# Optimization experiments

Measured on AMD Instinct MI355X. Metric: run time of the kernel, lower is better.

The kernel has to match this reference:

```python
import jax, jax.numpy as jnp
import numpy as np

N, E = 50000, 800000
D_IN, D_HID, D_OUT = 128, 256, 128


def setup_inputs() -> dict:
    key = jax.random.key(0)
    k = jax.random.split(key, 7)
    x = jax.random.normal(k[0], (N, D_IN), dtype=jnp.float32)
    edge_src = jax.random.randint(k[1], (E,), 0, N, dtype=jnp.int32)
    edge_dst = jax.random.randint(k[2], (E,), 0, N, dtype=jnp.int32)
    s1 = 1.0 / np.sqrt(2 * D_IN)
    s2 = 1.0 / np.sqrt(2 * D_HID)
    W1 = jax.random.uniform(k[3], (2 * D_IN, D_HID), jnp.float32, -s1, s1)
    b1 = jax.random.uniform(k[4], (D_HID,), jnp.float32, -s1, s1)
    W2 = jax.random.uniform(k[5], (2 * D_HID, D_OUT), jnp.float32, -s2, s2)
    b2 = jax.random.uniform(k[6], (D_OUT,), jnp.float32, -s2, s2)
    return {"x": x, "edge_src": edge_src, "edge_dst": edge_dst,
            "W1": W1, "b1": b1, "W2": W2, "b2": b2}


def _sage_layer(h, edge_src, edge_dst, W, b, inv_deg):
    # mean-pool neighbor features: gather [E, D] then segment-sum to [N, D]
    msgs = h[edge_src]
    agg = jax.ops.segment_sum(msgs, edge_dst, num_segments=h.shape[0]) * inv_deg
    y = jnp.concatenate([h, agg], axis=1)  # [N, 2D]
    return y @ W + b


def reference(x, edge_src, edge_dst, W1, b1, W2, b2):
    n = x.shape[0]
    deg = jax.ops.segment_sum(jnp.ones_like(edge_dst, dtype=x.dtype), edge_dst,
                              num_segments=n)
    inv_deg = (1.0 / jnp.maximum(deg, 1.0))[:, None]  # isolated nodes -> zeros
    h = _sage_layer(x, edge_src, edge_dst, W1, b1, inv_deg)
    h = jax.nn.relu(h)
    # dropout is identity in eval mode
    h = _sage_layer(h, edge_src, edge_dst, W2, b2, inv_deg)
    return jax.nn.log_softmax(h, axis=1)
```

## Files before the change

kernel.cpp:

```cpp
#include <hip/hip_runtime.h>
#include <cstdint>
#include <cstddef>

typedef __attribute__((ext_vector_type(8))) short bf16x8;
typedef __attribute__((ext_vector_type(4))) float f32x4;
typedef __attribute__((ext_vector_type(2))) float f32x2;

__device__ inline short bf16_rne(float f) {
  unsigned u = __builtin_bit_cast(unsigned, f);
  u += 0x7fff + ((u >> 16) & 1);
  return (short)(u >> 16);
}

__device__ inline float bf16lo(unsigned v) { return __builtin_bit_cast(float, v << 16); }
__device__ inline float bf16hi(unsigned v) { return __builtin_bit_cast(float, v & 0xffff0000u); }

__device__ inline unsigned pack2(float a, float b) {
  return ((unsigned)(unsigned short)bf16_rne(a)) | (((unsigned)(unsigned short)bf16_rne(b)) << 16);
}


__global__ __launch_bounds__(256) void prep_kernel(const float* __restrict__ W1,
                                                   const float* __restrict__ W2,
                                                   const float* __restrict__ b2,
                                                   const float* __restrict__ x,
                                                   short* __restrict__ B1p,
                                                   short* __restrict__ B2p,
                                                   float* __restrict__ bias2,
                                                   unsigned* __restrict__ A1u,
                                                   unsigned* __restrict__ xf8, int nquads,
                                                   int* __restrict__ counters, int NB) {
  int b = blockIdx.x;
  int tid = threadIdx.x;
  int nqb = (nquads + 255) >> 8;
  if (b < 512) {
    int mode = b >> 8;
    int idx = (b & 255) * 256 + tid;
    int j = idx & 7;
    int L = (idx >> 3) & 63;
    int nt = (idx >> 9) & 15;
    int kb = idx >> 13;
    int k = kb * 32 + (L >> 4) * 8 + j;
    int n = nt * 16 + (L & 15);
    if (mode == 0) {
      B1p[idx] = bf16_rne(W1[(size_t)k * 256 + n]);
    } else {
      float v = (n < 128) ? W2[(size_t)k * 128 + n] : W2[(size_t)(256 + k) * 128 + (n - 128)];
      B2p[idx] = bf16_rne(v);
    }
  } else if (b == 512) {
    bias2[tid] = (tid < 128) ? b2[tid] : 0.0f;
  } else if (b < 513 + nqb) {
    int idx = (b - 513) * 256 + tid;
    if (idx < nquads) {
      int n = idx >> 5, q = idx & 31;
      float4 v = ((const float4*)x)[idx];
      ((uint2*)A1u)[(size_t)n * 64 + q] = make_uint2(pack2(v.x, v.y), pack2(v.z, v.w));
      int pk = __builtin_amdgcn_cvt_pk_fp8_f32(v.x, v.y, 0, false);
      pk = __builtin_amdgcn_cvt_pk_fp8_f32(v.z, v.w, pk, true);
      xf8[(size_t)n * 32 + q] = (unsigned)pk;
    }
  } else {
    for (int t = tid; t < NB; t += 256) counters[t] = 0;
  }
}

__global__ __launch_bounds__(256) void bucket_scatter(const int* __restrict__ src,
                                                      const int* __restrict__ dst, int E, int EPB,
                                                      int* __restrict__ counters, int NB,
                                                      int SLACK, unsigned* __restrict__ bedge) {
  __shared__ int h[512];
  __shared__ int base[512];
  int tid = threadIdx.x;
  for (int t = tid; t < NB; t += 256) h[t] = 0;
  __syncthreads();
  int start = blockIdx.x * EPB, end = min(E, start + EPB);
  for (int i = start + tid; i < end; i += 256) atomicAdd(&h[((unsigned)dst[i]) >> 7], 1);
  __syncthreads();
  for (int t = tid; t < NB; t += 256) {
    int c = h[t];
    base[t] = (c > 0) ? atomicAdd(&counters[t], c) : 0;
    h[t] = 0;
  }
  __syncthreads();
  for (int i = start + tid; i < end; i += 256) {
    unsigned d = (unsigned)dst[i];
    unsigned bk = d >> 7;
    int p = base[bk] + atomicAdd(&h[bk], 1);
    bedge[(size_t)bk * SLACK + p] = ((d & 127u) << 24) | (unsigned)src[i];
  }
}

__global__ __launch_bounds__(256) void build_csr(const unsigned* __restrict__ bedge,
                                                 const int* __restrict__ counters,
                                                 int NB, int SLACK, int N,
                                                 int* __restrict__ offsets,
                                                 int* __restrict__ oend,
                                                 float* __restrict__ inv_deg,
                                                 int* __restrict__ ssrc) {
  __shared__ int buf[128];
  int b = blockIdx.x, tid = threadIdx.x;
  int cntE = counters[b];
  int rb = b * SLACK;
  if (tid < 128) buf[tid] = 0;
  __syncthreads();
  for (int i = tid; i < cntE; i += 256) atomicAdd(&buf[bedge[(size_t)rb + i] >> 24], 1);
  __syncthreads();
  int cnt = (tid < 128) ? buf[tid] : 0;
  #pragma unroll
  for (int off = 1; off < 128; off <<= 1) {
    int t = (tid >= off && tid < 128) ? buf[tid - off] : 0;
    __syncthreads();
    if (tid < 128) buf[tid] += t;
    __syncthreads();
  }
  if (tid < 128) {
    int excl_l = buf[tid] - cnt;
    int node = (b << 7) + tid;
    if (node < N) {
      offsets[node] = rb + excl_l;
      oend[node]    = rb + excl_l + cnt;
      inv_deg[node] = 1.0f / fmaxf((float)cnt, 1.0f);
    }
    buf[tid] = rb + excl_l;
  }
  __syncthreads();
  for (int i = tid; i < cntE; i += 256) {
    unsigned e2 = bedge[(size_t)rb + i];
    int p = atomicAdd(&buf[e2 >> 24], 1);
    ssrc[p] = (int)(e2 & 0xFFFFFFu);
  }
}

#define CVT8(U, A0, A1, A2, A3, A4, A5, A6, A7)                                        \
  {                                                                                    \
    f32x2 p_, q_;                                                                      \
    p_ = __builtin_amdgcn_cvt_pk_f32_fp8((U).x, false);                                \
    q_ = __builtin_amdgcn_cvt_pk_f32_fp8((U).x, true);                                 \
    A0 += p_[0]; A1 += p_[1]; A2 += q_[0]; A3 += q_[1];                                \
    p_ = __builtin_amdgcn_cvt_pk_f32_fp8((U).y, false);                                \
    q_ = __builtin_amdgcn_cvt_pk_f32_fp8((U).y, true);                                 \
    A4 += p_[0]; A5 += p_[1]; A6 += q_[0]; A7 += q_[1];                                \
  }

__global__ __launch_bounds__(256) void agg1_kernel(const uint2* __restrict__ X8,
                                                   const int* __restrict__ offsets,
                                                   const int* __restrict__ oend,
                                                   const int* __restrict__ ssrc,
                                                   const float* __restrict__ inv_deg,
                                                   uint4* __restrict__ A1q, int N) {
  int node = blockIdx.x * 4 + (threadIdx.x >> 6);
  if (node >= N) return;
  int lane = threadIdx.x & 63;
  int g = lane >> 4;
  int l = lane & 15;
  int s = offsets[node], e = oend[node];
  float a0=0.f,a1=0.f,a2=0.f,a3=0.f,a4=0.f,a5=0.f,a6=0.f,a7=0.f;
  int i = s;
  for (; i + 16 <= e; i += 16) {
    int sA = ssrc[i + g], sB = ssrc[i + 4 + g];
    int sC = ssrc[i + 8 + g], sD = ssrc[i + 12 + g];
    uint2 u = X8[((size_t)(unsigned)sA << 4) + l];
    uint2 v = X8[((size_t)(unsigned)sB << 4) + l];
    uint2 w = X8[((size_t)(unsigned)sC << 4) + l];
    uint2 z = X8[((size_t)(unsigned)sD << 4) + l];
    CVT8(u, a0,a1,a2,a3,a4,a5,a6,a7);
    CVT8(v, a0,a1,a2,a3,a4,a5,a6,a7);
    CVT8(w, a0,a1,a2,a3,a4,a5,a6,a7);
    CVT8(z, a0,a1,a2,a3,a4,a5,a6,a7);
  }
  for (; i < e; i += 4) {
    if (g < e - i) {
      uint2 u = X8[((size_t)(unsigned)ssrc[i + g] << 4) + l];
      CVT8(u, a0,a1,a2,a3,a4,a5,a6,a7);
    }
  }
  a0 += __shfl_xor(a0,16,64); a0 += __shfl_xor(a0,32,64);
  a1 += __shfl_xor(a1,16,64); a1 += __shfl_xor(a1,32,64);
  a2 += __shfl_xor(a2,16,64); a2 += __shfl_xor(a2,32,64);
  a3 += __shfl_xor(a3,16,64); a3 += __shfl_xor(a3,32,64);
  a4 += __shfl_xor(a4,16,64); a4 += __shfl_xor(a4,32,64);
  a5 += __shfl_xor(a5,16,64); a5 += __shfl_xor(a5,32,64);
  a6 += __shfl_xor(a6,16,64); a6 += __shfl_xor(a6,32,64);
  a7 += __shfl_xor(a7,16,64); a7 += __shfl_xor(a7,32,64);
  if (g == 0) {
    float id = inv_deg[node];
    A1q[((size_t)node << 5) + 16 + l] =
        make_uint4(pack2(a0 * id, a1 * id), pack2(a2 * id, a3 * id),
                   pack2(a4 * id, a5 * id), pack2(a6 * id, a7 * id));
  }
}

__global__ __launch_bounds__(256, 2) void gemm_mfma(const short* __restrict__ A,
                                                    const short* __restrict__ Bp,
                                                    const float* __restrict__ bias,
                                                    void* __restrict__ out0,
                                                    void* __restrict__ out1,
                                                    int S, int mode) {
  int tid = threadIdx.x;
  int w = tid >> 6;
  int lane = tid & 63;

  bf16x8 breg[8][4];
  #pragma unroll
  for (int kb = 0; kb < 8; ++kb)
    #pragma unroll
    for (int j = 0; j < 4; ++j)
      breg[kb][j] = *(const bf16x8*)(Bp + ((size_t)((kb * 16 + w * 4 + j) * 64 + lane)) * 8);

  float bj[4];
  #pragma unroll
  for (int j = 0; j < 4; ++j) bj[j] = bias[w * 64 + j * 16 + (lane & 15)];

  int rowInFrag = lane & 15;
  int kseg = (lane >> 4) * 8;

  for (int s = blockIdx.x; s < S; s += gridDim.x) {
    int row0 = s * 16;
    const short* Arow = A + (size_t)(row0 + rowInFrag) * 256 + kseg;
    bf16x8 afr[8];
    #pragma unroll
    for (int kb = 0; kb < 8; ++kb) afr[kb] = *(const bf16x8*)(Arow + kb * 32);

    f32x4 acc[4];
    #pragma unroll
    for (int j = 0; j < 4; ++j) acc[j] = (f32x4)(0.0f);
    #pragma unroll
    for (int kb = 0; kb < 8; ++kb)
      #pragma unroll
      for (int j = 0; j < 4; ++j)
        acc[j] = __builtin_amdgcn_mfma_f32_16x16x32_bf16(afr[kb], breg[kb][j], acc[j], 0, 0, 0);

    int crow0 = row0 + (lane >> 4) * 4;
    int ccol = lane & 15;
    #pragma unroll
    for (int j = 0; j < 4; ++j) {
      int col = w * 64 + j * 16 + ccol;
      #pragma unroll
      for (int r = 0; r < 4; ++r) {
        float v = acc[j][r] + bj[j];
        int row = crow0 + r;
        if (mode == 0) {
          ((short*)out0)[(size_t)row * 256 + col] = bf16_rne(fmaxf(v, 0.0f));
        } else if (w < 2) {
          ((short*)out0)[(size_t)row * 128 + col] = bf16_rne(v);
        } else {
          int pk = __builtin_amdgcn_cvt_pk_fp8_f32(v, v, 0, false);
          ((unsigned char*)out1)[(size_t)row * 128 + (col - 128)] = (unsigned char)(pk & 0xff);
        }
      }
    }
  }
}

__global__ __launch_bounds__(256) void final_kernel(const uint4* __restrict__ utopq,
                                                    const uint2* __restrict__ T2,
                                                    const int* __restrict__ offsets,
                                                    const int* __restrict__ oend,
                                                    const int* __restrict__ ssrc,
                                                    const float* __restrict__ inv_deg,
                                                    float4* __restrict__ out4, int N) {
  int node = blockIdx.x * 4 + (threadIdx.x >> 6);
  if (node >= N) return;
  int lane = threadIdx.x & 63;
  int g = lane >> 4;
  int l = lane & 15;
  int s = offsets[node], e = oend[node];
  float a0=0.f,a1=0.f,a2=0.f,a3=0.f,a4=0.f,a5=0.f,a6=0.f,a7=0.f;
  int i = s;
  for (; i + 16 <= e; i += 16) {
    int sA = ssrc[i + g], sB = ssrc[i + 4 + g];
    int sC = ssrc[i + 8 + g], sD = ssrc[i + 12 + g];
    uint2 u = T2[((size_t)(unsigned)sA << 4) + l];
    uint2 v = T2[((size_t)(unsigned)sB << 4) + l];
    uint2 w = T2[((size_t)(unsigned)sC << 4) + l];
    uint2 z = T2[((size_t)(unsigned)sD << 4) + l];
    CVT8(u, a0,a1,a2,a3,a4,a5,a6,a7);
    CVT8(v, a0,a1,a2,a3,a4,a5,a6,a7);
    CVT8(w, a0,a1,a2,a3,a4,a5,a6,a7);
    CVT8(z, a0,a1,a2,a3,a4,a5,a6,a7);
  }
  for (; i < e; i += 4) {
    if (g < e - i) {
      uint2 u = T2[((size_t)(unsigned)ssrc[i + g] << 4) + l];
      CVT8(u, a0,a1,a2,a3,a4,a5,a6,a7);
    }
  }
  a0 += __shfl_xor(a0,16,64); a0 += __shfl_xor(a0,32,64);
  a1 += __shfl_xor(a1,16,64); a1 += __shfl_xor(a1,32,64);
  a2 += __shfl_xor(a2,16,64); a2 += __shfl_xor(a2,32,64);
  a3 += __shfl_xor(a3,16,64); a3 += __shfl_xor(a3,32,64);
  a4 += __shfl_xor(a4,16,64); a4 += __shfl_xor(a4,32,64);
  a5 += __shfl_xor(a5,16,64); a5 += __shfl_xor(a5,32,64);
  a6 += __shfl_xor(a6,16,64); a6 += __shfl_xor(a6,32,64);
  a7 += __shfl_xor(a7,16,64); a7 += __shfl_xor(a7,32,64);
  if (g == 0) {
    float id = inv_deg[node];
    uint4 U = utopq[((size_t)node << 4) + l];
    float v0 = bf16lo(U.x) + a0 * id;
    float v1 = bf16hi(U.x) + a1 * id;
    float v2 = bf16lo(U.y) + a2 * id;
    float v3 = bf16hi(U.y) + a3 * id;
    float v4 = bf16lo(U.z) + a4 * id;
    float v5 = bf16hi(U.z) + a5 * id;
    float v6 = bf16lo(U.w) + a6 * id;
    float v7 = bf16hi(U.w) + a7 * id;
    float m = fmaxf(fmaxf(fmaxf(v0, v1), fmaxf(v2, v3)), fmaxf(fmaxf(v4, v5), fmaxf(v6, v7)));
    #pragma unroll
    for (int off = 1; off < 16; off <<= 1) m = fmaxf(m, __shfl_xor(m, off, 16));
    float su = expf(v0 - m) + expf(v1 - m) + expf(v2 - m) + expf(v3 - m) +
               expf(v4 - m) + expf(v5 - m) + expf(v6 - m) + expf(v7 - m);
    #pragma unroll
    for (int off = 1; off < 16; off <<= 1) su += __shfl_xor(su, off, 16);
    float ls = m + logf(su);
    out4[((size_t)node << 5) + l * 2]     = make_float4(v0 - ls, v1 - ls, v2 - ls, v3 - ls);
    out4[((size_t)node << 5) + l * 2 + 1] = make_float4(v4 - ls, v5 - ls, v6 - ls, v7 - ls);
  }
}

extern "C" void kernel_launch(void* const* d_in, const int* in_sizes, int n_in,
                              void* d_out, int out_size, void* d_ws, size_t ws_size,
                              hipStream_t stream) {
  const float* x        = (const float*)d_in[0];
  const int*   edge_src = (const int*)d_in[1];
  const int*   edge_dst = (const int*)d_in[2];
  const float* W1       = (const float*)d_in[3];
  const float* b1       = (const float*)d_in[4];
  const float* W2       = (const float*)d_in[5];
  const float* b2       = (const float*)d_in[6];
  float* out = (float*)d_out;

  const int D_IN = 128;
  const int N = in_sizes[0] / D_IN;
  const int E = in_sizes[1];
  const int M_pad = ((N + 127) / 128) * 128;

  const int SB = 512;
  const int EPB = (E + SB - 1) / SB;
  const int NB = (N + 127) >> 7;
  const int SLACK = 3072;

  char* ws = (char*)d_ws;
  size_t p = 0;
  auto take = [&](size_t bytes) -> size_t {
    size_t r = p;
    p += (bytes + 255) & ~(size_t)255;
    return r;
  };
  size_t cnt_off   = take((size_t)NB * 4);
  size_t bedge_off = take((size_t)NB * SLACK * 4);
  size_t offs_off  = take((size_t)N * 4);
  size_t oend_off  = take((size_t)N * 4);
  size_t inv_off   = take((size_t)N * 4);
  size_t ssrc_off  = take((size_t)NB * SLACK * 4);
  size_t A1_off    = take((size_t)M_pad * 256 * 2);
  size_t xf8_off   = take((size_t)M_pad * 128);
  size_t h_off     = take((size_t)M_pad * 256 * 2);
  size_t B1p_off   = take((size_t)256 * 256 * 2);
  size_t B2p_off   = take((size_t)256 * 256 * 2);
  size_t bias2_off = take((size_t)256 * 4);
  size_t utop_off  = take((size_t)M_pad * 128 * 2);
  size_t t2_off    = take((size_t)M_pad * 128);
  (void)ws_size;

  int*   counters = (int*)(ws + cnt_off);
  unsigned* bedge = (unsigned*)(ws + bedge_off);
  int*   offsets  = (int*)(ws + offs_off);
  int*   oendp    = (int*)(ws + oend_off);
  float* inv_deg  = (float*)(ws + inv_off);
  int*   ssrc     = (int*)(ws + ssrc_off);
  unsigned* A1u   = (unsigned*)(ws + A1_off);
  unsigned* xf8   = (unsigned*)(ws + xf8_off);
  short* h        = (short*)(ws + h_off);
  short* B1p      = (short*)(ws + B1p_off);
  short* B2p      = (short*)(ws + B2p_off);
  float* bias2    = (float*)(ws + bias2_off);
  short* utop     = (short*)(ws + utop_off);
  unsigned char* t2f8 = (unsigned char*)(ws + t2_off);

  {
    int nquads = N * 32;
    int grid = 513 + (nquads + 255) / 256 + 1;
    prep_kernel<<<grid, 256, 0, stream>>>(W1, W2, b2, x, B1p, B2p, bias2, A1u, xf8, nquads,
                                          counters, NB);
  }
  bucket_scatter<<<SB, 256, 0, stream>>>(edge_src, edge_dst, E, EPB, counters, NB, SLACK, bedge);
  build_csr<<<NB, 256, 0, stream>>>(bedge, counters, NB, SLACK, N, offsets, oendp, inv_deg, ssrc);

  agg1_kernel<<<(N + 3) / 4, 256, 0, stream>>>((const uint2*)xf8, offsets, oendp, ssrc, inv_deg,
                                               (uint4*)A1u, N);
  {
    int S = M_pad / 16;
    gemm_mfma<<<1024, 256, 0, stream>>>((const short*)A1u, B1p, b1, h, nullptr, S, 0);
    gemm_mfma<<<1024, 256, 0, stream>>>(h, B2p, bias2, utop, t2f8, S, 1);
  }
  final_kernel<<<(N + 3) / 4, 256, 0, stream>>>((const uint4*)utop, (const uint2*)t2f8,
                                                offsets, oendp, ssrc, inv_deg, (float4*)out, N);
}
```

Before: 221.4 us.

## Fuse prep, bucketing, CSR build and layer-1 aggregation into one persistent kernel

Merges four separate launches (prep, bucket scatter, CSR build, first aggregation) into a single persistent kernel of 1536 blocks. Phases run as grid-stride loops separated by a software grid barrier built on an atomic counter, which is reset with a memset before launch. The goal is to remove kernel launch gaps and tail effects between the small stages. In exchange it relies on all blocks being co-resident, since the barrier would deadlock otherwise, and it adds spin-wait barrier overhead between phases.

```diff
diff --git a/kernel.cpp b/kernel.cpp
--- a/kernel.cpp
+++ b/kernel.cpp
@@ -19,175 +19,185 @@
   return ((unsigned)(unsigned short)bf16_rne(a)) | (((unsigned)(unsigned short)bf16_rne(b)) << 16);
 }
 
-
-__global__ __launch_bounds__(256) void prep_kernel(const float* __restrict__ W1,
-                                                   const float* __restrict__ W2,
-                                                   const float* __restrict__ b2,
-                                                   const float* __restrict__ x,
-                                                   short* __restrict__ B1p,
-                                                   short* __restrict__ B2p,
-                                                   float* __restrict__ bias2,
-                                                   unsigned* __restrict__ A1u,
-                                                   unsigned* __restrict__ xf8, int nquads,
-                                                   int* __restrict__ counters, int NB) {
-  int b = blockIdx.x;
+__device__ inline void gsync(int* bar, int target) {
+  __syncthreads();
+  if (threadIdx.x == 0) {
+    __threadfence();
+    atomicAdd(bar, 1);
+    while (atomicAdd(bar, 0) < target) __builtin_amdgcn_s_sleep(2);
+    __threadfence();
+  }
+  __syncthreads();
+}
+
+__global__ __launch_bounds__(256, 6) void pipeline_kernel(
+    const float* __restrict__ W1, const float* __restrict__ W2,
+    const float* __restrict__ b2, const float* __restrict__ x,
+    short* __restrict__ B1p, short* __restrict__ B2p, float* __restrict__ bias2,
+    unsigned* __restrict__ A1u, unsigned* __restrict__ xf8, int nquads,
+    const int* __restrict__ esrc, const int* __restrict__ edst, int E, int EPB,
+    int* __restrict__ counters, int NB, int SLACK, unsigned* __restrict__ bedge, int SB,
+    int* __restrict__ offsets, int* __restrict__ oend, float* __restrict__ inv_deg,
+    int* __restrict__ ssrc, int N, int* __restrict__ bar) {
+  __shared__ int sm[1024];
   int tid = threadIdx.x;
+  int G = gridDim.x;
+
   int nqb = (nquads + 255) >> 8;
-  if (b < 512) {
-    int mode = b >> 8;
-    int idx = (b & 255) * 256 + tid;
-    int j = idx & 7;
-    int L = (idx >> 3) & 63;
-    int nt = (idx >> 9) & 15;
-    int kb = idx >> 13;
-    int k = kb * 32 + (L >> 4) * 8 + j;
-    int n = nt * 16 + (L & 15);
-    if (mode == 0) {
-      B1p[idx] = bf16_rne(W1[(size_t)k * 256 + n]);
+  int totalA = 513 + nqb + 1;
+  for (int b = blockIdx.x; b < totalA; b += G) {
+    if (b < 512) {
+      int mode = b >> 8;
+      int idx = (b & 255) * 256 + tid;
+      int j = idx & 7;
+      int L = (idx >> 3) & 63;
+      int nt = (idx >> 9) & 15;
+      int kb = idx >> 13;
+      int k = kb * 32 + (L >> 4) * 8 + j;
+      int n = nt * 16 + (L & 15);
+      if (mode == 0) {
+        B1p[idx] = bf16_rne(W1[(size_t)k * 256 + n]);
+      } else {
+        float v = (n < 128) ? W2[(size_t)k * 128 + n] : W2[(size_t)(256 + k) * 128 + (n - 128)];
+        B2p[idx] = bf16_rne(v);
+      }
+    } else if (b == 512) {
+      bias2[tid] = (tid < 128) ? b2[tid] : 0.0f;
+    } else if (b < 513 + nqb) {
+      int idx = (b - 513) * 256 + tid;
+      if (idx < nquads) {
+        int n = idx >> 5, q = idx & 31;
+        float4 v = ((const float4*)x)[idx];
+        ((uint2*)A1u)[(size_t)n * 64 + q] = make_uint2(pack2(v.x, v.y), pack2(v.z, v.w));
+        int pk = __builtin_amdgcn_cvt_pk_fp8_f32(v.x, v.y, 0, false);
+        pk = __builtin_amdgcn_cvt_pk_fp8_f32(v.z, v.w, pk, true);
+        xf8[(size_t)n * 32 + q] = (unsigned)pk;
+      }
     } else {
-      float v = (n < 128) ? W2[(size_t)k * 128 + n] : W2[(size_t)(256 + k) * 128 + (n - 128)];
-      B2p[idx] = bf16_rne(v);
-    }
-  } else if (b == 512) {
-    bias2[tid] = (tid < 128) ? b2[tid] : 0.0f;
-  } else if (b < 513 + nqb) {
-    int idx = (b - 513) * 256 + tid;
-    if (idx < nquads) {
-      int n = idx >> 5, q = idx & 31;
-      float4 v = ((const float4*)x)[idx];
-      ((uint2*)A1u)[(size_t)n * 64 + q] = make_uint2(pack2(v.x, v.y), pack2(v.z, v.w));
-      int pk = __builtin_amdgcn_cvt_pk_fp8_f32(v.x, v.y, 0, false);
-      pk = __builtin_amdgcn_cvt_pk_fp8_f32(v.z, v.w, pk, true);
-      xf8[(size_t)n * 32 + q] = (unsigned)pk;
-    }
-  } else {
-    for (int t = tid; t < NB; t += 256) counters[t] = 0;
-  }
-}
-
-__global__ __launch_bounds__(256) void bucket_scatter(const int* __restrict__ src,
-                                                      const int* __restrict__ dst, int E, int EPB,
-                                                      int* __restrict__ counters, int NB,
-                                                      int SLACK, unsigned* __restrict__ bedge) {
-  __shared__ int h[512];
-  __shared__ int base[512];
-  int tid = threadIdx.x;
-  for (int t = tid; t < NB; t += 256) h[t] = 0;
-  __syncthreads();
-  int start = blockIdx.x * EPB, end = min(E, start + EPB);
-  for (int i = start + tid; i < end; i += 256) atomicAdd(&h[((unsigned)dst[i]) >> 7], 1);
-  __syncthreads();
-  for (int t = tid; t < NB; t += 256) {
-    int c = h[t];
-    base[t] = (c > 0) ? atomicAdd(&counters[t], c) : 0;
-    h[t] = 0;
-  }
-  __syncthreads();
-  for (int i = start + tid; i < end; i += 256) {
-    unsigned d = (unsigned)dst[i];
-    unsigned bk = d >> 7;
-    int p = base[bk] + atomicAdd(&h[bk], 1);
-    bedge[(size_t)bk * SLACK + p] = ((d & 127u) << 24) | (unsigned)src[i];
-  }
-}
-
-__global__ __launch_bounds__(256) void build_csr(const unsigned* __restrict__ bedge,
-                                                 const int* __restrict__ counters,
-                                                 int NB, int SLACK, int N,
-                                                 int* __restrict__ offsets,
-                                                 int* __restrict__ oend,
-                                                 float* __restrict__ inv_deg,
-                                                 int* __restrict__ ssrc) {
-  __shared__ int buf[128];
-  int b = blockIdx.x, tid = threadIdx.x;
-  int cntE = counters[b];
-  int rb = b * SLACK;
-  if (tid < 128) buf[tid] = 0;
-  __syncthreads();
-  for (int i = tid; i < cntE; i += 256) atomicAdd(&buf[bedge[(size_t)rb + i] >> 24], 1);
-  __syncthreads();
-  int cnt = (tid < 128) ? buf[tid] : 0;
-  #pragma unroll
-  for (int off = 1; off < 128; off <<= 1) {
-    int t = (tid >= off && tid < 128) ? buf[tid - off] : 0;
-    __syncthreads();
-    if (tid < 128) buf[tid] += t;
-    __syncthreads();
-  }
-  if (tid < 128) {
-    int excl_l = buf[tid] - cnt;
-    int node = (b << 7) + tid;
-    if (node < N) {
-      offsets[node] = rb + excl_l;
-      oend[node]    = rb + excl_l + cnt;
-      inv_deg[node] = 1.0f / fmaxf((float)cnt, 1.0f);
-    }
-    buf[tid] = rb + excl_l;
-  }
-  __syncthreads();
-  for (int i = tid; i < cntE; i += 256) {
-    unsigned e2 = bedge[(size_t)rb + i];
-    int p = atomicAdd(&buf[e2 >> 24], 1);
-    ssrc[p] = (int)(e2 & 0xFFFFFFu);
-  }
-}
-
-#define CVT8(U, A0, A1, A2, A3, A4, A5, A6, A7)                                        \
-  {                                                                                    \
-    f32x2 p_, q_;                                                                      \
-    p_ = __builtin_amdgcn_cvt_pk_f32_fp8((U).x, false);                                \
-    q_ = __builtin_amdgcn_cvt_pk_f32_fp8((U).x, true);                                 \
-    A0 += p_[0]; A1 += p_[1]; A2 += q_[0]; A3 += q_[1];                                \
-    p_ = __builtin_amdgcn_cvt_pk_f32_fp8((U).y, false);                                \
-    q_ = __builtin_amdgcn_cvt_pk_f32_fp8((U).y, true);                                 \
-    A4 += p_[0]; A5 += p_[1]; A6 += q_[0]; A7 += q_[1];                                \
-  }
-
-__global__ __launch_bounds__(256) void agg1_kernel(const uint2* __restrict__ X8,
-                                                   const int* __restrict__ offsets,
-                                                   const int* __restrict__ oend,
-                                                   const int* __restrict__ ssrc,
-                                                   const float* __restrict__ inv_deg,
-                                                   uint4* __restrict__ A1q, int N) {
-  int node = blockIdx.x * 4 + (threadIdx.x >> 6);
-  if (node >= N) return;
-  int lane = threadIdx.x & 63;
-  int g = lane >> 4;
+      for (int t = tid; t < NB; t += 256) counters[t] = 0;
+    }
+  }
+  gsync(bar, G);
+
+  for (int b = blockIdx.x; b < SB; b += G) {
+    int* h = sm;
+    int* base = sm + 512;
+    for (int t = tid; t < NB; t += 256) h[t] = 0;
+    __syncthreads();
+    int start = b * EPB, end = min(E, start + EPB);
+    for (int i = start + tid; i < end; i += 256) atomicAdd(&h[((unsigned)edst[i]) >> 7], 1);
+    __syncthreads();
+    for (int t = tid; t < NB; t += 256) {
+      int c = h[t];
+      base[t] = (c > 0) ? atomicAdd(&counters[t], c) : 0;
+      h[t] = 0;
+    }
+    __syncthreads();
+    for (int i = start + tid; i < end; i += 256) {
+      unsigned d = (unsigned)edst[i];
+      unsigned bk = d >> 7;
+      int p = base[bk] + atomicAdd(&h[bk], 1);
+      bedge[(size_t)bk * SLACK + p] = ((d & 127u) << 24) | (unsigned)esrc[i];
+    }
+    __syncthreads();
+  }
+  gsync(bar, 2 * G);
+
+  for (int b = blockIdx.x; b < NB; b += G) {
+    int* buf = sm;
+    int cntE = counters[b];
+    int rb = b * SLACK;
+    if (tid < 128) buf[tid] = 0;
+    __syncthreads();
+    for (int i = tid; i < cntE; i += 256) atomicAdd(&buf[bedge[(size_t)rb + i] >> 24], 1);
+    __syncthreads();
+    int cnt = (tid < 128) ? buf[tid] : 0;
+    #pragma unroll
+    for (int off = 1; off < 128; off <<= 1) {
+      int t = (tid >= off && tid < 128) ? buf[tid - off] : 0;
+      __syncthreads();
+      if (tid < 128) buf[tid] += t;
+      __syncthreads();
+    }
+    if (tid < 128) {
+      int excl_l = buf[tid] - cnt;
+      int node = (b << 7) + tid;
+      if (node < N) {
+        offsets[node] = rb + excl_l;
+        oend[node]    = rb + excl_l + cnt;
+        inv_deg[node] = 1.0f / fmaxf((float)cnt, 1.0f);
+      }
+      buf[tid] = rb + excl_l;
+    }
+    __syncthreads();
+    for (int i = tid; i < cntE; i += 256) {
+      unsigned e2 = bedge[(size_t)rb + i];
+      int p = atomicAdd(&buf[e2 >> 24], 1);
+      ssrc[p] = (int)(e2 & 0xFFFFFFu);
+    }
+    __syncthreads();
+  }
+  gsync(bar, 3 * G);
+
+  int ngrp = (N + 3) >> 2;
+  int lane = tid & 63;
+  int lg = lane >> 4;
   int l = lane & 15;
-  int s = offsets[node], e = oend[node];
-  float a0=0.f,a1=0.f,a2=0.f,a3=0.f,a4=0.f,a5=0.f,a6=0.f,a7=0.f;
-  int i = s;
-  for (; i + 16 <= e; i += 16) {
-    int sA = ssrc[i + g], sB = ssrc[i + 4 + g];
-    int sC = ssrc[i + 8 + g], sD = ssrc[i + 12 + g];
-    uint2 u = X8[((size_t)(unsigned)sA << 4) + l];
-    uint2 v = X8[((size_t)(unsigned)sB << 4) + l];
-    uint2 w = X8[((size_t)(unsigned)sC << 4) + l];
-    uint2 z = X8[((size_t)(unsigned)sD << 4) + l];
-    CVT8(u, a0,a1,a2,a3,a4,a5,a6,a7);
-    CVT8(v, a0,a1,a2,a3,a4,a5,a6,a7);
-    CVT8(w, a0,a1,a2,a3,a4,a5,a6,a7);
-    CVT8(z, a0,a1,a2,a3,a4,a5,a6,a7);
-  }
-  for (; i < e; i += 4) {
-    if (g < e - i) {
-      uint2 u = X8[((size_t)(unsigned)ssrc[i + g] << 4) + l];
-      CVT8(u, a0,a1,a2,a3,a4,a5,a6,a7);
-    }
-  }
-  a0 += __shfl_xor(a0,16,64); a0 += __shfl_xor(a0,32,64);
-  a1 += __shfl_xor(a1,16,64); a1 += __shfl_xor(a1,32,64);
-  a2 += __shfl_xor(a2,16,64); a2 += __shfl_xor(a2,32,64);
-  a3 += __shfl_xor(a3,16,64); a3 += __shfl_xor(a3,32,64);
-  a4 += __shfl_xor(a4,16,64); a4 += __shfl_xor(a4,32,64);
-  a5 += __shfl_xor(a5,16,64); a5 += __shfl_xor(a5,32,64);
-  a6 += __shfl_xor(a6,16,64); a6 += __shfl_xor(a6,32,64);
-  a7 += __shfl_xor(a7,16,64); a7 += __shfl_xor(a7,32,64);
-  if (g == 0) {
-    float id = inv_deg[node];
-    A1q[((size_t)node << 5) + 16 + l] =
-        make_uint4(pack2(a0 * id, a1 * id), pack2(a2 * id, a3 * id),
-                   pack2(a4 * id, a5 * id), pack2(a6 * id, a7 * id));
+  for (int grp = blockIdx.x; grp < ngrp; grp += G) {
+    int node = grp * 4 + (tid >> 6);
+    if (node >= N) continue;
+    int s = offsets[node], e = oend[node];
+    float a0=0.f,a1=0.f,a2=0.f,a3=0.f,a4=0.f,a5=0.f,a6=0.f,a7=0.f;
+    int i = s;
+    for (; i + 16 <= e; i += 16) {
+      int sA = ssrc[i + lg], sB = ssrc[i + 4 + lg];
+      int sC = ssrc[i + 8 + lg], sD = ssrc[i + 12 + lg];
+      uint2 u = ((const uint2*)xf8)[((size_t)(unsigned)sA << 4) + l];
+      uint2 v = ((const uint2*)xf8)[((size_t)(unsigned)sB << 4) + l];
+      uint2 w = ((const uint2*)xf8)[((size_t)(unsigned)sC << 4) + l];
+      uint2 z = ((const uint2*)xf8)[((size_t)(unsigned)sD << 4) + l];
+      f32x2 p_, q_;
+      p_ = __builtin_amdgcn_cvt_pk_f32_fp8(u.x, false); q_ = __builtin_amdgcn_cvt_pk_f32_fp8(u.x, true);
+      a0 += p_[0]; a1 += p_[1]; a2 += q_[0]; a3 += q_[1];
+      p_ = __builtin_amdgcn_cvt_pk_f32_fp8(u.y, false); q_ = __builtin_amdgcn_cvt_pk_f32_fp8(u.y, true);
+      a4 += p_[0]; a5 += p_[1]; a6 += q_[0]; a7 += q_[1];
+      p_ = __builtin_amdgcn_cvt_pk_f32_fp8(v.x, false); q_ = __builtin_amdgcn_cvt_pk_f32_fp8(v.x, true);
+      a0 += p_[0]; a1 += p_[1]; a2 += q_[0]; a3 += q_[1];
+      p_ = __builtin_amdgcn_cvt_pk_f32_fp8(v.y, false); q_ = __builtin_amdgcn_cvt_pk_f32_fp8(v.y, true);
+      a4 += p_[0]; a5 += p_[1]; a6 += q_[0]; a7 += q_[1];
+      p_ = __builtin_amdgcn_cvt_pk_f32_fp8(w.x, false); q_ = __builtin_amdgcn_cvt_pk_f32_fp8(w.x, true);
+      a0 += p_[0]; a1 += p_[1]; a2 += q_[0]; a3 += q_[1];
+      p_ = __builtin_amdgcn_cvt_pk_f32_fp8(w.y, false); q_ = __builtin_amdgcn_cvt_pk_f32_fp8(w.y, true);
+      a4 += p_[0]; a5 += p_[1]; a6 += q_[0]; a7 += q_[1];
+      p_ = __builtin_amdgcn_cvt_pk_f32_fp8(z.x, false); q_ = __builtin_amdgcn_cvt_pk_f32_fp8(z.x, true);
+      a0 += p_[0]; a1 += p_[1]; a2 += q_[0]; a3 += q_[1];
+      p_ = __builtin_amdgcn_cvt_pk_f32_fp8(z.y, false); q_ = __builtin_amdgcn_cvt_pk_f32_fp8(z.y, true);
+      a4 += p_[0]; a5 += p_[1]; a6 += q_[0]; a7 += q_[1];
+    }
+    for (; i < e; i += 4) {
+      if (lg < e - i) {
+        uint2 u = ((const uint2*)xf8)[((size_t)(unsigned)ssrc[i + lg] << 4) + l];
+        f32x2 p_, q_;
+        p_ = __builtin_amdgcn_cvt_pk_f32_fp8(u.x, false); q_ = __builtin_amdgcn_cvt_pk_f32_fp8(u.x, true);
+        a0 += p_[0]; a1 += p_[1]; a2 += q_[0]; a3 += q_[1];
+        p_ = __builtin_amdgcn_cvt_pk_f32_fp8(u.y, false); q_ = __builtin_amdgcn_cvt_pk_f32_fp8(u.y, true);
+        a4 += p_[0]; a5 += p_[1]; a6 += q_[0]; a7 += q_[1];
+      }
+    }
+    a0 += __shfl_xor(a0,16,64); a0 += __shfl_xor(a0,32,64);
+    a1 += __shfl_xor(a1,16,64); a1 += __shfl_xor(a1,32,64);
+    a2 += __shfl_xor(a2,16,64); a2 += __shfl_xor(a2,32,64);
+    a3 += __shfl_xor(a3,16,64); a3 += __shfl_xor(a3,32,64);
+    a4 += __shfl_xor(a4,16,64); a4 += __shfl_xor(a4,32,64);
+    a5 += __shfl_xor(a5,16,64); a5 += __shfl_xor(a5,32,64);
+    a6 += __shfl_xor(a6,16,64); a6 += __shfl_xor(a6,32,64);
+    a7 += __shfl_xor(a7,16,64); a7 += __shfl_xor(a7,32,64);
+    if (lg == 0) {
+      float id = inv_deg[node];
+      ((uint4*)A1u)[((size_t)node << 5) + 16 + l] =
+          make_uint4(pack2(a0 * id, a1 * id), pack2(a2 * id, a3 * id),
+                     pack2(a4 * id, a5 * id), pack2(a6 * id, a7 * id));
+    }
   }
 }
 
@@ -252,6 +262,17 @@
     }
   }
 }
+
+#define CVT8(U, A0, A1, A2, A3, A4, A5, A6, A7)                                        \
+  {                                                                                    \
+    f32x2 p_, q_;                                                                      \
+    p_ = __builtin_amdgcn_cvt_pk_f32_fp8((U).x, false);                                \
+    q_ = __builtin_amdgcn_cvt_pk_f32_fp8((U).x, true);                                 \
+    A0 += p_[0]; A1 += p_[1]; A2 += q_[0]; A3 += q_[1];                                \
+    p_ = __builtin_amdgcn_cvt_pk_f32_fp8((U).y, false);                                \
+    q_ = __builtin_amdgcn_cvt_pk_f32_fp8((U).y, true);                                 \
+    A4 += p_[0]; A5 += p_[1]; A6 += q_[0]; A7 += q_[1];                                \
+  }
 
 __global__ __launch_bounds__(256) void final_kernel(const uint4* __restrict__ utopq,
                                                     const uint2* __restrict__ T2,
@@ -339,6 +360,7 @@
   const int EPB = (E + SB - 1) / SB;
   const int NB = (N + 127) >> 7;
   const int SLACK = 3072;
+  const int GRID = 1536;
 
   char* ws = (char*)d_ws;
   size_t p = 0;
@@ -347,6 +369,7 @@
     p += (bytes + 255) & ~(size_t)255;
     return r;
   };
+  size_t bar_off   = take(256);
   size_t cnt_off   = take((size_t)NB * 4);
   size_t bedge_off = take((size_t)NB * SLACK * 4);
   size_t offs_off  = take((size_t)N * 4);
@@ -363,6 +386,7 @@
   size_t t2_off    = take((size_t)M_pad * 128);
   (void)ws_size;
 
+  int*   bar      = (int*)(ws + bar_off);
   int*   counters = (int*)(ws + cnt_off);
   unsigned* bedge = (unsigned*)(ws + bedge_off);
   int*   offsets  = (int*)(ws + offs_off);
@@ -378,17 +402,14 @@
   short* utop     = (short*)(ws + utop_off);
   unsigned char* t2f8 = (unsigned char*)(ws + t2_off);
 
+  hipMemsetAsync(bar, 0, 4, stream);
+
   {
     int nquads = N * 32;
-    int grid = 513 + (nquads + 255) / 256 + 1;
-    prep_kernel<<<grid, 256, 0, stream>>>(W1, W2, b2, x, B1p, B2p, bias2, A1u, xf8, nquads,
-                                          counters, NB);
-  }
-  bucket_scatter<<<SB, 256, 0, stream>>>(edge_src, edge_dst, E, EPB, counters, NB, SLACK, bedge);
-  build_csr<<<NB, 256, 0, stream>>>(bedge, counters, NB, SLACK, N, offsets, oendp, inv_deg, ssrc);
-
-  agg1_kernel<<<(N + 3) / 4, 256, 0, stream>>>((const uint2*)xf8, offsets, oendp, ssrc, inv_deg,
-                                               (uint4*)A1u, N);
+    pipeline_kernel<<<GRID, 256, 0, stream>>>(W1, W2, b2, x, B1p, B2p, bias2, A1u, xf8, nquads,
+                                              edge_src, edge_dst, E, EPB, counters, NB, SLACK,
+                                              bedge, SB, offsets, oendp, inv_deg, ssrc, N, bar);
+  }
   {
     int S = M_pad / 16;
     gemm_mfma<<<1024, 256, 0, stream>>>((const short*)A1u, B1p, b1, h, nullptr, S, 0);
```

New measurement: 685.0 us. 3.09x slower.
